# Performance work log

Measured on AMD Instinct MI355X. Metric: run time of the kernel, lower is better.

## Reference

```python
import jax, jax.numpy as jnp
import numpy as np

N, E, DIN, DH, DOUT, NB = 50000, 400000, 32, 128, 16, 2

def setup_inputs() -> dict:
    key = jax.random.key(0)
    ks = jax.random.split(key, 16)
    s = 0.05
    inp = {
        "inputs": jax.random.normal(ks[0], (N, DIN), jnp.float32),
        "frames": jax.random.normal(ks[1], (N, 3, 3), jnp.float32),
        "edge_index": jax.random.randint(ks[2], (2, E), 0, N, jnp.int32),
        # GraphNet in/out projections
        "win": jax.random.normal(ks[3], (DIN, DH), jnp.float32) * s,
        "bin_": jnp.zeros((DH,), jnp.float32),
        "wout": jax.random.normal(ks[4], (DH, DOUT), jnp.float32) * s,
        "bout": jnp.zeros((DOUT,), jnp.float32),
        # per-block EdgeConv params, stacked over NB blocks
        # mlp1: Linear(2*DH, DH) -> ReLU -> Linear(DH, DH) -> ReLU -> Linear(DH, DH)
        "w1a": jax.random.normal(ks[5], (NB, 2 * DH, DH), jnp.float32) * s,
        "b1a": jnp.zeros((NB, DH), jnp.float32),
        "w1b": jax.random.normal(ks[6], (NB, DH, DH), jnp.float32) * s,
        "b1b": jnp.zeros((NB, DH), jnp.float32),
        "w1c": jax.random.normal(ks[7], (NB, DH, DH), jnp.float32) * s,
        "b1c": jnp.zeros((NB, DH), jnp.float32),
        # mlp2: Linear(DH, DH) -> ReLU -> Linear(DH, DH)
        "w2a": jax.random.normal(ks[8], (NB, DH, DH), jnp.float32) * s,
        "b2a": jnp.zeros((NB, DH), jnp.float32),
        "w2b": jax.random.normal(ks[9], (NB, DH, DH), jnp.float32) * s,
        "b2b": jnp.zeros((NB, DH), jnp.float32),
    }
    return inp


def reference(inputs, frames, edge_index, win, bin_, wout, bout,
              w1a, b1a, w1b, b1b, w1c, b1c, w2a, b2a, w2b, b2b):
    src = edge_index[0]  # j: message source
    dst = edge_index[1]  # i: aggregation target (PyG convention)
    x = inputs @ win + bin_  # [N, DH]
    for b in range(NB):
        x_j = x[src]  # [E, DH] gather
        x_i = x[dst]  # [E, DH] gather
        m = jnp.concatenate([x_j, x_i], axis=-1)  # [E, 2*DH]
        m = jax.nn.relu(m @ w1a[b] + b1a[b])
        m = jax.nn.relu(m @ w1b[b] + b1b[b])
        m = m @ w1c[b] + b1c[b]  # [E, DH]
        agg = jax.ops.segment_sum(m, dst, num_segments=N)  # aggr='add'
        h = jax.nn.relu(agg @ w2a[b] + b2a[b])
        x = h @ w2b[b] + b2b[b]
    return x @ wout + bout  # [N, DOUT]
```

## Files before the change

kernel.cpp:

```cpp
#include <hip/hip_runtime.h>

#define NN 50000
#define NE 400000
#define DIN 32
#define DH  128
#define DOUT 16
#define NB  2
#define NBLK 49
#define NTILE (NE / 64)
#define TPW   5
#define NWG_E (NTILE / TPW)

typedef _Float16 half8 __attribute__((ext_vector_type(8)));
typedef _Float16 half4 __attribute__((ext_vector_type(4)));
typedef float    f32x4 __attribute__((ext_vector_type(4)));

#define FENCE() asm volatile("s_waitcnt lgkmcnt(0)" ::: "memory")
#define MFMA16(a, b, c) __builtin_amdgcn_mfma_f32_16x16x32_f16((a), (b), (c), 0, 0, 0)

__global__ void k_prep(const float* __restrict__ w1a, const float* __restrict__ w1b,
                       const float* __restrict__ w1c, const float* __restrict__ w2a,
                       const float* __restrict__ w2b, const float* __restrict__ wout,
                       const float* __restrict__ win, const int* __restrict__ dstI,
                       _Float16* __restrict__ wf, int* __restrict__ deg) {
    const int b = blockIdx.x, tid = threadIdx.x;
    if (b < (NB * 12288) / 256) {
        int c = b * 256 + tid;
        int bb = c / 12288, r = c % 12288;
        int tt = r >> 9, rem = r & 511;
        const float* W; int t;
        if (tt < 8)       { W = w1a + (size_t)bb * 2 * DH * DH; t = tt; }
        else if (tt < 12) { W = w1b + (size_t)bb * DH * DH; t = tt - 8; }
        else if (tt < 16) { W = w1c + (size_t)bb * DH * DH; t = tt - 12; }
        else if (tt < 20) { W = w2a + (size_t)bb * DH * DH; t = tt - 16; }
        else              { W = w2b + (size_t)bb * DH * DH; t = tt - 20; }
        bool perm = (tt >= 12 && tt < 16);
        int n = rem >> 6, l = rem & 63;
        int col = n * 16 + (l & 15);
        half8 v;
#pragma unroll
        for (int j = 0; j < 8; ++j) {
            int row = perm ? ((2 * t + (j >> 2)) * 16 + (l >> 4) * 4 + (j & 3))
                           : (t * 32 + (l >> 4) * 8 + j);
            v[j] = (_Float16)W[(size_t)row * DH + col];
        }
        *(half8*)(wf + (size_t)c * 8) = v;
    } else if (b == 96) {
        int c = tid;
        int t = c >> 6, l = c & 63;
        half8 v;
#pragma unroll
        for (int j = 0; j < 8; ++j)
            v[j] = (_Float16)wout[(size_t)(t * 32 + (l >> 4) * 8 + j) * DOUT + (l & 15)];
        *(half8*)(wf + (size_t)(NB * 12288 + c) * 8) = v;
    } else if (b < 99) {
        int c = (b - 97) * 256 + tid;
        int n = c >> 6, l = c & 63;
        half8 v;
#pragma unroll
        for (int j = 0; j < 8; ++j)
            v[j] = (_Float16)win[(size_t)((l >> 4) * 8 + j) * DH + n * 16 + (l & 15)];
        *(half8*)(wf + (size_t)(NB * 12288 + 256 + c) * 8) = v;
    } else {
        int e = (b - 99) * 256 + tid;
        if (e < NE) atomicAdd(&deg[dstI[e]], 1);
    }
}

__global__ void __launch_bounds__(1024) k_scanA(const int* __restrict__ deg,
                                                int* __restrict__ bsum) {
    __shared__ int ws[16];
    int tid = threadIdx.x, wv = tid >> 6, l = tid & 63;
    int i = blockIdx.x * 1024 + tid;
    int v = (i < NN) ? deg[i] : 0;
#pragma unroll
    for (int off = 32; off; off >>= 1) v += __shfl_down(v, off);
    if (l == 0) ws[wv] = v;
    __syncthreads();
    if (tid == 0) {
        int s = 0;
#pragma unroll
        for (int k = 0; k < 16; ++k) s += ws[k];
        bsum[blockIdx.x] = s;
    }
}

__global__ void k_scanB(const int* __restrict__ bsum, int* __restrict__ boff) {
    int l = threadIdx.x;
    int v = (l < NBLK) ? bsum[l] : 0;
    int s = v;
#pragma unroll
    for (int off = 1; off < 64; off <<= 1) {
        int t = __shfl_up(s, off);
        if (l >= off) s += t;
    }
    if (l < NBLK) boff[l] = s - v;
}

__global__ void __launch_bounds__(1024) k_scanC(const int* __restrict__ deg,
                                                const int* __restrict__ boff,
                                                int* __restrict__ cur) {
    __shared__ int ws[16];
    int tid = threadIdx.x, wv = tid >> 6, l = tid & 63;
    int i = blockIdx.x * 1024 + tid;
    int v = (i < NN) ? deg[i] : 0;
    int s = v;
#pragma unroll
    for (int off = 1; off < 64; off <<= 1) {
        int t = __shfl_up(s, off);
        if (l >= off) s += t;
    }
    if (l == 63) ws[wv] = s;
    __syncthreads();
    if (wv == 0) {
        int t = (l < 16) ? ws[l] : 0;
#pragma unroll
        for (int off = 1; off < 16; off <<= 1) {
            int u = __shfl_up(t, off);
            if (l >= off) t += u;
        }
        if (l < 16) ws[l] = t;
    }
    __syncthreads();
    int base = boff[blockIdx.x] + (wv ? ws[wv - 1] : 0);
    if (i < NN) cur[i] = base + s - v;
}

__global__ void k_scatter(const int* __restrict__ srcI, const int* __restrict__ dstI,
                          int* __restrict__ cur, int* __restrict__ eS,
                          int* __restrict__ eD) {
    int e = blockIdx.x * blockDim.x + threadIdx.x;
    if (e >= NE) return;
    int d = dstI[e];
    int p = atomicAdd(&cur[d], 1);
    eS[p] = srcI[e];
    eD[p] = d;
}

__global__ void __launch_bounds__(256, 4) k_y0(
    const float* __restrict__ inp,
    const half8* __restrict__ winf, const float* __restrict__ bin,
    const half8* __restrict__ wfa, const float* __restrict__ b1a,
    _Float16* __restrict__ yj, _Float16* __restrict__ yi,
    float* __restrict__ agg) {
    __shared__ _Float16 sM[4][2048];
    const int tid = threadIdx.x, wv = tid >> 6, l = tid & 63;
    const int lm = l & 15, lk = l >> 4;
    const int n0 = (blockIdx.x * 4 + wv) * 16;
    if (n0 >= NN) return;
    int node = n0 + lm;
    if (node >= NN) node = NN - 1;

    {
        float4 z4 = make_float4(0.f, 0.f, 0.f, 0.f);
#pragma unroll
        for (int r = 0; r < 4; ++r) {
            int nd = n0 + lk * 4 + r;
            if (nd < NN) {
                float4* q = (float4*)(agg + (size_t)nd * DH + lm * 8);
                q[0] = z4; q[1] = z4;
            }
        }
    }

    const f32x4 z = {0.f, 0.f, 0.f, 0.f};
    half8 a0;
    {
        const float* ip = inp + (size_t)node * DIN + lk * 8;
        float4 v0 = *(const float4*)ip;
        float4 v1 = *(const float4*)(ip + 4);
#pragma unroll
        for (int j = 0; j < 4; ++j) {
            a0[j]     = (_Float16)(&v0.x)[j];
            a0[4 + j] = (_Float16)(&v1.x)[j];
        }
    }
    f32x4 xacc[8];
#pragma unroll
    for (int n = 0; n < 8; ++n) xacc[n] = z;
#pragma unroll
    for (int n = 0; n < 8; ++n) xacc[n] = MFMA16(a0, winf[n * 64 + l], xacc[n]);

    _Float16* sm = sM[wv];
#pragma unroll
    for (int n = 0; n < 8; ++n) {
        float bi = bin[n * 16 + lm];
        int base = ((n >> 1) * 64 + ((n & 1) * 2 + (lm >> 3)) * 16 + lk * 4) * 8 +
                   (lm & 7);
#pragma unroll
        for (int j = 0; j < 4; ++j)
            sm[base + j * 8] = (_Float16)(xacc[n][j] + bi);
    }
    FENCE();

    f32x4 aj[8], ai[8];
#pragma unroll
    for (int n = 0; n < 8; ++n) { aj[n] = z; ai[n] = z; }
#pragma unroll
    for (int t = 0; t < 4; ++t) {
        half8 a = *(const half8*)&sm[(t * 64 + l) * 8];
#pragma unroll
        for (int n = 0; n < 8; ++n) {
            aj[n] = MFMA16(a, wfa[(size_t)(t * 8 + n) * 64 + l], aj[n]);
            ai[n] = MFMA16(a, wfa[(size_t)((t + 4) * 8 + n) * 64 + l], ai[n]);
        }
    }
#pragma unroll
    for (int n = 0; n < 8; ++n) {
        float bi = b1a[n * 16 + lm];
#pragma unroll
        for (int r = 0; r < 4; ++r) {
            int nd = n0 + lk * 4 + r;
            if (nd < NN) {
                yj[(size_t)nd * DH + n * 16 + lm] = (_Float16)aj[n][r];
                yi[(size_t)nd * DH + n * 16 + lm] = (_Float16)(ai[n][r] + bi);
            }
        }
    }
}

__global__ void __launch_bounds__(256, 2) k_edge12(
    const _Float16* __restrict__ yj, const _Float16* __restrict__ yi,
    const int* __restrict__ eS, const int* __restrict__ eD,
    const half8* __restrict__ wfb, const half8* __restrict__ wfc,
    const float* __restrict__ b1b,
    float* __restrict__ agg) {
    __shared__ _Float16 smAll[4][4096];
    __shared__ int slotT[4][16];

    const int tid = threadIdx.x, wv = tid >> 6, l = tid & 63;
    const int lm = l & 15, lk = l >> 4;

    int bid = blockIdx.x;
    int xcd = bid & 7, idx = bid >> 3;
    int wg = (xcd < 2 ? xcd * 157 : 2 * 157 + (xcd - 2) * 156) + idx;
    const int ebase0 = (wg * TPW) * 64 + wv * 16;

    _Float16* sm = smAll[wv];
    if (lk >= 2) {
        half8 zz;
#pragma unroll
        for (int j = 0; j < 8; ++j) zz[j] = (_Float16)0.f;
#pragma unroll
        for (int g = 0; g < 8; ++g) *(half8*)&sm[(g * 64 + l) * 8] = zz;
    }

    half4 bb[8];
#pragma unroll
    for (int n = 0; n < 8; ++n) {
        float4 bf = *(const float4*)(b1b + n * 16 + lk * 4);
#pragma unroll
        for (int r = 0; r < 4; ++r) bb[n][r] = (_Float16)(&bf.x)[r];
    }

    const f32x4 z = {0.f, 0.f, 0.f, 0.f};

    int src = eS[ebase0 + lm];
    int dst = eD[ebase0 + lm];
    half8 ya0, ya1, ya2, ya3, yb0, yb1, yb2, yb3;
    ya0 = *(const half8*)(yj + (size_t)src * DH + 0 * 32 + lk * 8);
    ya1 = *(const half8*)(yj + (size_t)src * DH + 1 * 32 + lk * 8);
    ya2 = *(const half8*)(yj + (size_t)src * DH + 2 * 32 + lk * 8);
    ya3 = *(const half8*)(yj + (size_t)src * DH + 3 * 32 + lk * 8);
    yb0 = *(const half8*)(yi + (size_t)dst * DH + 0 * 32 + lk * 8);
    yb1 = *(const half8*)(yi + (size_t)dst * DH + 1 * 32 + lk * 8);
    yb2 = *(const half8*)(yi + (size_t)dst * DH + 2 * 32 + lk * 8);
    yb3 = *(const half8*)(yi + (size_t)dst * DH + 3 * 32 + lk * 8);

#pragma unroll
    for (int i = 0; i < TPW; ++i) {
        const int ebase = ebase0 + i * 64;

        int srcN = 0, dstN = 0;
        if (i + 1 < TPW) {
            srcN = eS[ebase + 64 + lm];
            dstN = eD[ebase + 64 + lm];
        }

        int dprev = __shfl(dst, (l & 48) | ((lm - 1) & 15));
        bool bit = (lm == 0) || (dst != dprev);
        unsigned mask16 = (unsigned)__ballot(bit) & 0xFFFFu;
        int slot_l = __popc(mask16 & ((2u << lm) - 1)) - 1;
        int nsl = __popc(mask16);
        if (l < 16 && bit) slotT[wv][slot_l] = dst;

        f32x4 acc[8];
#pragma unroll
        for (int n = 0; n < 8; ++n) acc[n] = z;
        {
            half8 m1;
#pragma unroll
            for (int j = 0; j < 8; ++j) {
                _Float16 v = ya0[j] + yb0[j];
                m1[j] = v > (_Float16)0.f ? v : (_Float16)0.f;
            }
#pragma unroll
            for (int n = 0; n < 8; ++n)
                acc[n] = MFMA16(wfb[(size_t)(0 * 8 + n) * 64 + l], m1, acc[n]);
#pragma unroll
            for (int j = 0; j < 8; ++j) {
                _Float16 v = ya1[j] + yb1[j];
                m1[j] = v > (_Float16)0.f ? v : (_Float16)0.f;
            }
#pragma unroll
            for (int n = 0; n < 8; ++n)
                acc[n] = MFMA16(wfb[(size_t)(1 * 8 + n) * 64 + l], m1, acc[n]);
#pragma unroll
            for (int j = 0; j < 8; ++j) {
                _Float16 v = ya2[j] + yb2[j];
                m1[j] = v > (_Float16)0.f ? v : (_Float16)0.f;
            }
#pragma unroll
            for (int n = 0; n < 8; ++n)
                acc[n] = MFMA16(wfb[(size_t)(2 * 8 + n) * 64 + l], m1, acc[n]);
#pragma unroll
            for (int j = 0; j < 8; ++j) {
                _Float16 v = ya3[j] + yb3[j];
                m1[j] = v > (_Float16)0.f ? v : (_Float16)0.f;
            }
#pragma unroll
            for (int n = 0; n < 8; ++n)
                acc[n] = MFMA16(wfb[(size_t)(3 * 8 + n) * 64 + l], m1, acc[n]);
        }

        if (i + 1 < TPW) {
            ya0 = *(const half8*)(yj + (size_t)srcN * DH + 0 * 32 + lk * 8);
            ya1 = *(const half8*)(yj + (size_t)srcN * DH + 1 * 32 + lk * 8);
            ya2 = *(const half8*)(yj + (size_t)srcN * DH + 2 * 32 + lk * 8);
            ya3 = *(const half8*)(yj + (size_t)srcN * DH + 3 * 32 + lk * 8);
            yb0 = *(const half8*)(yi + (size_t)dstN * DH + 0 * 32 + lk * 8);
            yb1 = *(const half8*)(yi + (size_t)dstN * DH + 1 * 32 + lk * 8);
            yb2 = *(const half8*)(yi + (size_t)dstN * DH + 2 * 32 + lk * 8);
            yb3 = *(const half8*)(yi + (size_t)dstN * DH + 3 * 32 + lk * 8);
        }

        f32x4 ac3[8];
#pragma unroll
        for (int n = 0; n < 8; ++n) ac3[n] = z;
#pragma unroll
        for (int t = 0; t < 4; ++t) {
            half8 b3;
#pragma unroll
            for (int j = 0; j < 8; ++j) {
                int n2 = 2 * t + (j >> 2), r = j & 3;
                float v = acc[n2][r] + (float)bb[n2][r];
                b3[j] = (_Float16)fmaxf(v, 0.f);
            }
#pragma unroll
            for (int n = 0; n < 8; ++n)
                ac3[n] = MFMA16(wfc[(size_t)(t * 8 + n) * 64 + l], b3, ac3[n]);
        }

#pragma unroll
        for (int n = 0; n < 8; ++n)
#pragma unroll
            for (int r = 0; r < 4; ++r)
                sm[(n * 64 + (lm >> 3) * 16 + lk * 4 + r) * 8 + (lm & 7)] =
                    (_Float16)ac3[n][r];
        FENCE();

        half8 ind;
#pragma unroll
        for (int e8 = 0; e8 < 8; ++e8) {
            int ks = lk * 8 + e8;
            int se = __shfl(slot_l, ks & 15);
            ind[e8] = (ks < 16 && se == lm) ? (_Float16)1.f : (_Float16)0.f;
        }
        int4 dv = *(const int4*)&slotT[wv][lk * 4];
#pragma unroll
        for (int g = 0; g < 8; ++g) {
            half8 bf = *(const half8*)&sm[(g * 64 + l) * 8];
            f32x4 p = MFMA16(ind, bf, z);
#pragma unroll
            for (int r = 0; r < 4; ++r) {
                int s0 = lk * 4 + r;
                if (s0 < nsl)
                    unsafeAtomicAdd(agg + (size_t)(&dv.x)[r] * DH + g * 16 + lm, p[r]);
            }
        }

        src = srcN; dst = dstN;
    }
}

template <int MODE>
__global__ void __launch_bounds__(256, 3) k_node10(
    float* __restrict__ agg, const int* __restrict__ deg,
    const float* __restrict__ b1c,
    const half8* __restrict__ w2af, const half8* __restrict__ w2bf,
    const float* __restrict__ b2a, const float* __restrict__ b2b,
    const half8* __restrict__ wfaN, const float* __restrict__ b1aN,
    _Float16* __restrict__ yj, _Float16* __restrict__ yi,
    const half8* __restrict__ woutf, const float* __restrict__ bout,
    float* __restrict__ out) {
    __shared__ _Float16 sM[4][2048];
    const int tid = threadIdx.x, wv = tid >> 6, l = tid & 63;
    const int lm = l & 15, lk = l >> 4;
    const int n0 = (blockIdx.x * 4 + wv) * 16;
    if (n0 >= NN) return;
    int nodeA = n0 + lm;
    if (nodeA >= NN) nodeA = NN - 1;
    const float degf = (float)deg[nodeA];

    float b2ar[8], b2br[8];
#pragma unroll
    for (int n = 0; n < 8; ++n) {
        b2ar[n] = b2a[n * 16 + lm];
        b2br[n] = b2b[n * 16 + lm];
    }

    const f32x4 z = {0.f, 0.f, 0.f, 0.f};
    f32x4 acc[8];
#pragma unroll
    for (int n = 0; n < 8; ++n) acc[n] = z;

    for (int t = 0; t < 4; ++t) {
        float* ap = agg + (size_t)nodeA * DH + t * 32 + lk * 8;
        float4 v0 = *(const float4*)ap;
        float4 v1 = *(const float4*)(ap + 4);
        if (MODE == 0) {
            float4 z4 = make_float4(0.f, 0.f, 0.f, 0.f);
            *(float4*)ap = z4;
            *(float4*)(ap + 4) = z4;
        }
        float4 c0 = *(const float4*)(b1c + t * 32 + lk * 8);
        float4 c1 = *(const float4*)(b1c + t * 32 + lk * 8 + 4);
        half8 a;
#pragma unroll
        for (int j = 0; j < 4; ++j) {
            a[j]     = (_Float16)((&v0.x)[j] + degf * (&c0.x)[j]);
            a[4 + j] = (_Float16)((&v1.x)[j] + degf * (&c1.x)[j]);
        }
        const half8* wp = w2af + (size_t)t * 512 + l;
#pragma unroll
        for (int n = 0; n < 8; ++n) acc[n] = MFMA16(a, wp[n * 64], acc[n]);
    }
    _Float16* sm = sM[wv];
#pragma unroll
    for (int n = 0; n < 8; ++n) {
        int base = ((n >> 1) * 64 + ((n & 1) * 2 + (lm >> 3)) * 16 + lk * 4) * 8 +
                   (lm & 7);
#pragma unroll
        for (int j = 0; j < 4; ++j)
            sm[base + j * 8] = (_Float16)fmaxf(acc[n][j] + b2ar[n], 0.f);
    }
    FENCE();
#pragma unroll
    for (int n = 0; n < 8; ++n) acc[n] = z;
    for (int t = 0; t < 4; ++t) {
        half8 a = *(const half8*)&sm[(t * 64 + l) * 8];
        const half8* wp = w2bf + (size_t)t * 512 + l;
#pragma unroll
        for (int n = 0; n < 8; ++n) acc[n] = MFMA16(a, wp[n * 64], acc[n]);
    }
    FENCE();
#pragma unroll
    for (int n = 0; n < 8; ++n) {
        int base = ((n >> 1) * 64 + ((n & 1) * 2 + (lm >> 3)) * 16 + lk * 4) * 8 +
                   (lm & 7);
#pragma unroll
        for (int j = 0; j < 4; ++j)
            sm[base + j * 8] = (_Float16)(acc[n][j] + b2br[n]);
    }
    FENCE();

    if (MODE == 0) {
        f32x4 aj[8], ai[8];
#pragma unroll
        for (int n = 0; n < 8; ++n) { aj[n] = z; ai[n] = z; }
#pragma unroll
        for (int t = 0; t < 4; ++t) {
            half8 a = *(const half8*)&sm[(t * 64 + l) * 8];
#pragma unroll
            for (int n = 0; n < 8; ++n) {
                aj[n] = MFMA16(a, wfaN[(size_t)(t * 8 + n) * 64 + l], aj[n]);
                ai[n] = MFMA16(a, wfaN[(size_t)((t + 4) * 8 + n) * 64 + l], ai[n]);
            }
        }
#pragma unroll
        for (int n = 0; n < 8; ++n) {
            float bi = b1aN[n * 16 + lm];
#pragma unroll
            for (int r = 0; r < 4; ++r) {
                int nd = n0 + lk * 4 + r;
                if (nd < NN) {
                    yj[(size_t)nd * DH + n * 16 + lm] = (_Float16)aj[n][r];
                    yi[(size_t)nd * DH + n * 16 + lm] = (_Float16)(ai[n][r] + bi);
                }
            }
        }
    } else {
        f32x4 ao = z;
        for (int t = 0; t < 4; ++t) {
            half8 a = *(const half8*)&sm[(t * 64 + l) * 8];
            ao = MFMA16(a, woutf[t * 64 + l], ao);
        }
        float bo = bout[lm];
#pragma unroll
        for (int j = 0; j < 4; ++j) {
            int nd = n0 + lk * 4 + j;
            if (nd < NN) out[(size_t)nd * DOUT + lm] = ao[j] + bo;
        }
    }
}

extern "C" void kernel_launch(void* const* d_in, const int* in_sizes, int n_in,
                              void* d_out, int out_size, void* d_ws, size_t ws_size,
                              hipStream_t stream) {
    const float* inputs = (const float*)d_in[0];
    const int* eidx = (const int*)d_in[2];
    const int* srcI = eidx;
    const int* dstI = eidx + NE;
    const float* win  = (const float*)d_in[3];
    const float* bin_ = (const float*)d_in[4];
    const float* wout = (const float*)d_in[5];
    const float* bout = (const float*)d_in[6];
    const float* w1a = (const float*)d_in[7];
    const float* b1a = (const float*)d_in[8];
    const float* w1b = (const float*)d_in[9];
    const float* b1b = (const float*)d_in[10];
    const float* w1c = (const float*)d_in[11];
    const float* b1c = (const float*)d_in[12];
    const float* w2a = (const float*)d_in[13];
    const float* b2a = (const float*)d_in[14];
    const float* w2b = (const float*)d_in[15];
    const float* b2b = (const float*)d_in[16];

    char* p = (char*)d_ws;
    _Float16* yj = (_Float16*)p;    p += (size_t)NN * DH * 2;
    _Float16* yi = (_Float16*)p;    p += (size_t)NN * DH * 2;
    _Float16* wfAll = (_Float16*)p; p += ((size_t)NB * 12288 + 768) * 16;
    float* agg   = (float*)p;       p += (size_t)NN * DH * 4;
    int* deg     = (int*)p;         p += (size_t)NN * 4;
    int* cur     = (int*)p;         p += (size_t)NN * 4;
    int* bsum    = (int*)p;         p += 256;
    int* boff    = (int*)p;         p += 256;
    int* eSrt    = (int*)p;         p += (size_t)NE * 4;
    int* eDrt    = (int*)p;         p += (size_t)NE * 4;
    float* out   = (float*)d_out;

    const half8* wb0 = (const half8*)wfAll;
    const half8* wb1 = (const half8*)(wfAll + (size_t)12288 * 8);
    const half8* wfW = (const half8*)(wfAll + (size_t)NB * 12288 * 8);
    const half8* wfI = (const half8*)(wfAll + (size_t)(NB * 12288 + 256) * 8);

    hipMemsetAsync(deg, 0, (size_t)NN * 4, stream);
    k_prep<<<99 + (NE + 255) / 256, 256, 0, stream>>>(
        w1a, w1b, w1c, w2a, w2b, wout, win, dstI, wfAll, deg);
    k_scanA<<<NBLK, 1024, 0, stream>>>(deg, bsum);
    k_scanB<<<1, 64, 0, stream>>>(bsum, boff);
    k_scanC<<<NBLK, 1024, 0, stream>>>(deg, boff, cur);
    k_scatter<<<(NE + 255) / 256, 256, 0, stream>>>(srcI, dstI, cur, eSrt, eDrt);

    const int NWGN = (NN + 63) / 64;
    k_y0<<<NWGN, 256, 0, stream>>>(inputs, wfI, bin_, wb0, b1a, yj, yi, agg);
    k_edge12<<<NWG_E, 256, 0, stream>>>(yj, yi, eSrt, eDrt,
                                        wb0 + 4096, wb0 + 6144, b1b, agg);
    k_node10<0><<<NWGN, 256, 0, stream>>>(
        agg, deg, b1c, wb0 + 8192, wb0 + 10240, b2a, b2b,
        wb1, b1a + DH, yj, yi, nullptr, nullptr, nullptr);
    k_edge12<<<NWG_E, 256, 0, stream>>>(yj, yi, eSrt, eDrt,
                                        wb1 + 4096, wb1 + 6144, b1b + DH, agg);
    k_node10<1><<<NWGN, 256, 0, stream>>>(
        agg, deg, b1c + DH, wb1 + 8192, wb1 + 10240, b2a + DH, b2b + DH,
        nullptr, nullptr, nullptr, nullptr, wfW, bout, out);
}
```

Baseline: 309.7 us.

## Give each wave a contiguous edge range and carry segment sums across tiles

Each wave now handles 80 consecutive edges, five 16-edge tiles, instead of tiles strided 64 edges apart. The last dst segment of each tile is carried in registers into the next tile and merged when the dst matches. Segments that lie wholly inside a wave's range are written with plain stores, and only the boundary segments use atomic adds. This cuts atomic traffic on agg but depends on the edges being sorted by dst, and adds shuffle and branch work per tile.

```diff
diff --git a/kernel.cpp b/kernel.cpp
--- a/kernel.cpp
+++ b/kernel.cpp
@@ -9,7 +9,7 @@
 #define NBLK 49
 #define NTILE (NE / 64)
 #define TPW   5
-#define NWG_E (NTILE / TPW)
+#define NWG_E (NE / 320)
 
 typedef _Float16 half8 __attribute__((ext_vector_type(8)));
 typedef _Float16 half4 __attribute__((ext_vector_type(4)));
@@ -234,7 +234,7 @@
     int bid = blockIdx.x;
     int xcd = bid & 7, idx = bid >> 3;
     int wg = (xcd < 2 ? xcd * 157 : 2 * 157 + (xcd - 2) * 156) + idx;
-    const int ebase0 = (wg * TPW) * 64 + wv * 16;
+    const int ebase0 = wg * 320 + wv * 80;
 
     _Float16* sm = smAll[wv];
     if (lk >= 2) {
@@ -254,6 +254,12 @@
     }
 
     const f32x4 z = {0.f, 0.f, 0.f, 0.f};
+
+    float c8[8];
+#pragma unroll
+    for (int g = 0; g < 8; ++g) c8[g] = 0.f;
+    int carry_dst = -1;
+    bool carry_first = false;
 
     int src = eS[ebase0 + lm];
     int dst = eD[ebase0 + lm];
@@ -269,20 +275,36 @@
 
 #pragma unroll
     for (int i = 0; i < TPW; ++i) {
-        const int ebase = ebase0 + i * 64;
+        const int ebase = ebase0 + i * 16;
 
         int srcN = 0, dstN = 0;
         if (i + 1 < TPW) {
-            srcN = eS[ebase + 64 + lm];
-            dstN = eD[ebase + 64 + lm];
-        }
-
+            srcN = eS[ebase + 16 + lm];
+            dstN = eD[ebase + 16 + lm];
+        }
+
+        int slot0dst = __shfl(dst, 0);
         int dprev = __shfl(dst, (l & 48) | ((lm - 1) & 15));
         bool bit = (lm == 0) || (dst != dprev);
         unsigned mask16 = (unsigned)__ballot(bit) & 0xFFFFu;
         int slot_l = __popc(mask16 & ((2u << lm) - 1)) - 1;
         int nsl = __popc(mask16);
         if (l < 16 && bit) slotT[wv][slot_l] = dst;
+
+        const bool merge = (i > 0) && (slot0dst == carry_dst);
+        if (i > 0 && !merge) {
+            float* ap = agg + (size_t)carry_dst * DH + lm;
+            if (lk == 0) {
+                if (carry_first) {
+#pragma unroll
+                    for (int g = 0; g < 8; ++g)
+                        unsafeAtomicAdd(ap + g * 16, c8[g]);
+                } else {
+#pragma unroll
+                    for (int g = 0; g < 8; ++g) ap[g * 16] = c8[g];
+                }
+            }
+        }
 
         f32x4 acc[8];
 #pragma unroll
@@ -367,19 +389,45 @@
             ind[e8] = (ks < 16 && se == lm) ? (_Float16)1.f : (_Float16)0.f;
         }
         int4 dv = *(const int4*)&slotT[wv][lk * 4];
+        const int lkLast = (nsl - 1) >> 2, rLast = (nsl - 1) & 3;
+        const int newCarryDst = slotT[wv][nsl - 1];
+        const bool slot0_atomic = (i == 0) || (merge && carry_first);
+        float c8n[8];
 #pragma unroll
         for (int g = 0; g < 8; ++g) {
-            half8 bf = *(const half8*)&sm[(g * 64 + l) * 8];
-            f32x4 p = MFMA16(ind, bf, z);
+            half8 bfr = *(const half8*)&sm[(g * 64 + l) * 8];
+            f32x4 cseed = z;
+            if (merge && lk == 0) cseed[0] = c8[g];
+            f32x4 p = MFMA16(ind, bfr, cseed);
 #pragma unroll
             for (int r = 0; r < 4; ++r) {
                 int s0 = lk * 4 + r;
-                if (s0 < nsl)
-                    unsafeAtomicAdd(agg + (size_t)(&dv.x)[r] * DH + g * 16 + lm, p[r]);
-            }
-        }
+                if (s0 < nsl - 1) {
+                    float* ap = agg + (size_t)(&dv.x)[r] * DH + g * 16 + lm;
+                    if (s0 == 0 && slot0_atomic) unsafeAtomicAdd(ap, p[r]);
+                    else *ap = p[r];
+                }
+            }
+            float cand = (lk == lkLast)
+                ? (rLast == 0 ? p[0] : rLast == 1 ? p[1] : rLast == 2 ? p[2] : p[3])
+                : 0.f;
+            c8n[g] = __shfl(cand, lkLast * 16 + lm);
+        }
+#pragma unroll
+        for (int g = 0; g < 8; ++g) c8[g] = c8n[g];
+        carry_dst = newCarryDst;
+        carry_first = (i == 0) ? (nsl == 1)
+                               : (merge && (nsl == 1) && carry_first);
 
         src = srcN; dst = dstN;
+    }
+
+    {
+        float* ap = agg + (size_t)carry_dst * DH + lm;
+        if (lk == 0) {
+#pragma unroll
+            for (int g = 0; g < 8; ++g) unsafeAtomicAdd(ap + g * 16, c8[g]);
+        }
     }
 }
 
```

Result: slower. 338.4 us (+9.3%).
